# Optimization experiments

Measured on AMD Instinct MI355X. Metric: run time of the kernel, lower is better.

## Reference

```python
import jax, jax.numpy as jnp
import numpy as np

C, S, D, H, FF = 8, 512, 512, 8, 2048
DH = D // H
N = C * S
NUM_SAMPLES = 4
SEG_LEN = N // NUM_SAMPLES  # 2 channels * 512 tokens per sample


def _ln(x, w, b):
    m = x.mean(-1, keepdims=True)
    v = ((x - m) ** 2).mean(-1, keepdims=True)
    return (x - m) / jnp.sqrt(v + 1e-5) * w + b


def _rope_1d(t, p, inv_freq):
    # t: (H, N, hd), p: (N,), inv_freq: (hd//2,)
    f = p[:, None] * inv_freq[None, :]          # (N, hd//2)
    emb = jnp.concatenate([f, f], -1)           # (N, hd)
    cos, sin = jnp.cos(emb), jnp.sin(emb)
    half = t.shape[-1] // 2
    rot = jnp.concatenate([-t[..., half:], t[..., :half]], -1)
    return t * cos + rot * sin


def setup_inputs() -> dict:
    key = jax.random.key(0)
    ks = jax.random.split(key, 8)
    s = 0.02
    return {
        "x": jax.random.normal(ks[0], (C, S, D), jnp.float32),
        "pos": jax.random.uniform(ks[1], (C, S, 2), jnp.float32) * 100.0,
        "mask": jnp.zeros((C, S), jnp.bool_),
        "seg_ids": jnp.arange(N, dtype=jnp.int32),
        "Wqkv": jax.random.normal(ks[2], (D, 3 * D), jnp.float32) * s,
        "bqkv": jnp.zeros((3 * D,), jnp.float32),
        "Wo": jax.random.normal(ks[3], (D, D), jnp.float32) * s,
        "bo": jnp.zeros((D,), jnp.float32),
        "ln1_w": jnp.ones((D,), jnp.float32),
        "ln1_b": jnp.zeros((D,), jnp.float32),
        "ln2_w": jnp.ones((D,), jnp.float32),
        "ln2_b": jnp.zeros((D,), jnp.float32),
        "W1": jax.random.normal(ks[4], (D, FF), jnp.float32) * s,
        "b1": jnp.zeros((FF,), jnp.float32),
        "W2": jax.random.normal(ks[5], (FF, D), jnp.float32) * s,
        "b2": jnp.zeros((D,), jnp.float32),
    }


def reference(x, pos, mask, seg_ids, Wqkv, bqkv, Wo, bo,
              ln1_w, ln1_b, ln2_w, ln2_b, W1, b1, W2, b2):
    # Zero-mask forward_cc path: all C*S tokens are packed into one varlen batch.
    xf = x.reshape(N, D)
    pf = pos.reshape(N, 2)
    seg = seg_ids // SEG_LEN  # segment id per token (cu_seq_len semantics)

    # --- pre-LN MHA with 2D axial RoPE ---
    hn = _ln(xf, ln1_w, ln1_b)
    qkv = hn @ Wqkv + bqkv
    q, k, v = jnp.split(qkv, 3, axis=-1)
    to_heads = lambda t: t.reshape(N, H, DH).transpose(1, 0, 2)  # (H, N, DH)
    q, k, v = to_heads(q), to_heads(k), to_heads(v)

    hd2 = DH // 2
    inv_freq = 1.0 / (10000.0 ** (jnp.arange(0, hd2, 2, dtype=jnp.float32) / hd2))

    def rope2d(t):
        a = _rope_1d(t[..., :hd2], pf[:, 0], inv_freq)
        b = _rope_1d(t[..., hd2:], pf[:, 1], inv_freq)
        return jnp.concatenate([a, b], -1)

    q, k = rope2d(q), rope2d(k)

    scores = jnp.einsum('hnd,hmd->hnm', q, k) / np.float32(np.sqrt(DH))
    allowed = seg[:, None] == seg[None, :]  # block-diagonal varlen mask
    scores = jnp.where(allowed[None], scores, jnp.float32(-1e30))
    attn = jax.nn.softmax(scores, axis=-1)
    o = jnp.einsum('hnm,hmd->hnd', attn, v).transpose(1, 0, 2).reshape(N, D)
    h = xf + (o @ Wo + bo)

    # --- pre-LN FFN ---
    hn2 = _ln(h, ln2_w, ln2_b)
    h = h + (jax.nn.gelu(hn2 @ W1 + b1) @ W2 + b2)
    return h.reshape(C, S, D)
```

## Files before the change

kernel.cpp:

```cpp
#include <hip/hip_runtime.h>
#include <hip/hip_bf16.h>


typedef __hip_bfloat16 bf16;
typedef float f4 __attribute__((ext_vector_type(4)));
typedef short short8 __attribute__((ext_vector_type(8)));

#define C_ 8
#define S_ 512
#define D_ 512
#define H_ 8
#define DH_ 64
#define FF_ 2048
#define N_ 4096
#define SEGLEN 1024

__device__ __forceinline__ float bfbits2f(unsigned short u) {
    return __uint_as_float(((unsigned)u) << 16);
}
__device__ __forceinline__ unsigned short f2bfbits(float f) {
    __hip_bfloat16 h = __float2bfloat16(f);
    return *reinterpret_cast<unsigned short*>(&h);
}
__device__ __forceinline__ float in_get(const void* p, int i, int isbf) {
    return isbf ? bfbits2f(((const unsigned short*)p)[i]) : ((const float*)p)[i];
}
__device__ __forceinline__ int probe_bf(const void* ln1w) {
    return ((const unsigned*)ln1w)[0] != 0x3F800000u;
}
__device__ __forceinline__ float gelu_f(float x) {
    float u = 0.7978845608028654f * fmaf(0.044715f * x, x * x, x);
    return x * __builtin_amdgcn_rcpf(1.0f + __expf(-2.0f * u));
}
__device__ __forceinline__ void gl2lds16(const void* g, void* l) {
    __builtin_amdgcn_global_load_lds(
        (const __attribute__((address_space(1))) void*)g,
        (__attribute__((address_space(3))) void*)l, 16, 0, 0);
}

__device__ __forceinline__ void ln_row(
    const void* in, const void* w, const void* b, unsigned short* out,
    int isbf, int row, int lane, int in_fp32)
{
    int base = row * D_ + lane * 8;
    float v[8];
    if (in_fp32 || !isbf) {
        const f4* p = (const f4*)((const float*)in + base);
        f4 x0 = p[0], x1 = p[1];
        v[0] = x0[0]; v[1] = x0[1]; v[2] = x0[2]; v[3] = x0[3];
        v[4] = x1[0]; v[5] = x1[1]; v[6] = x1[2]; v[7] = x1[3];
    } else {
        uint4 u = *(const uint4*)((const unsigned short*)in + base);
        unsigned uu[4] = {u.x, u.y, u.z, u.w};
        #pragma unroll
        for (int j = 0; j < 4; j++) {
            v[2 * j]     = __uint_as_float(uu[j] << 16);
            v[2 * j + 1] = __uint_as_float(uu[j] & 0xFFFF0000u);
        }
    }
    float s = 0.f, q = 0.f;
    #pragma unroll
    for (int j = 0; j < 8; j++) { s += v[j]; q = fmaf(v[j], v[j], q); }
    #pragma unroll
    for (int m = 32; m; m >>= 1) { s += __shfl_xor(s, m); q += __shfl_xor(q, m); }
    float mean = s * (1.f / D_);
    float var  = q * (1.f / D_) - mean * mean;
    float rstd = rsqrtf(var + 1e-5f);
    unsigned short o[8];
    #pragma unroll
    for (int j = 0; j < 8; j++) {
        float wj = in_get(w, lane * 8 + j, isbf);
        float bj = in_get(b, lane * 8 + j, isbf);
        o[j] = f2bfbits((v[j] - mean) * rstd * wj + bj);
    }
    uint4 uo;
    uo.x = o[0] | ((unsigned)o[1] << 16);
    uo.y = o[2] | ((unsigned)o[3] << 16);
    uo.z = o[4] | ((unsigned)o[5] << 16);
    uo.w = o[6] | ((unsigned)o[7] << 16);
    *(uint4*)(out + base) = uo;
}

__device__ __forceinline__ void wtile_transpose(
    const void* __restrict__ src, bf16* __restrict__ dst, int K, int N,
    int nt, int kt, int isbf, unsigned short* t2)
{
    int nb = nt * 64, kb = kt * 32;
    #pragma unroll
    for (int pass = 0; pass < 2; pass++) {
        int k = pass * 16 + (threadIdx.x >> 4);
        int n = (threadIdx.x & 15) * 4;
        size_t gidx = (size_t)(kb + k) * N + nb + n;
        unsigned short v[4];
        if (!isbf) {
            f4 xv = *(const f4*)((const float*)src + gidx);
            v[0] = f2bfbits(xv[0]); v[1] = f2bfbits(xv[1]);
            v[2] = f2bfbits(xv[2]); v[3] = f2bfbits(xv[3]);
        } else {
            ushort4 u = *(const ushort4*)((const unsigned short*)src + gidx);
            v[0] = u.x; v[1] = u.y; v[2] = u.z; v[3] = u.w;
        }
        #pragma unroll
        for (int e = 0; e < 4; e++) t2[(n + e) * 40 + k] = v[e];
    }
    __syncthreads();
    int n = threadIdx.x >> 2, kc = (threadIdx.x & 3) * 8;
    uint4 w = *(const uint4*)&t2[n * 40 + kc];
    *(uint4*)&((unsigned short*)dst)[(size_t)(nb + n) * K + kb + kc] = w;
}

__global__ __launch_bounds__(256) void prep_kernel(
    const void* __restrict__ Wqkv, bf16* __restrict__ WqkvT,
    const void* __restrict__ x, const void* __restrict__ ln1w,
    const void* __restrict__ ln1b, unsigned short* __restrict__ hn)
{
    const int isbf = probe_bf(ln1w);
    __shared__ unsigned short t2[64 * 40];
    int b = blockIdx.x;
    if (b < 384) {
        wtile_transpose(Wqkv, WqkvT, 512, 1536, b % 24, b / 24, isbf, t2);
    } else {
        int row = (b - 384) * 4 + (threadIdx.x >> 6);
        ln_row(x, ln1w, ln1b, hn, isbf, row, threadIdx.x & 63, 0);
    }
}

__global__ __launch_bounds__(256) void ln_kernel(
    const void* __restrict__ in, const void* __restrict__ w, const void* __restrict__ b,
    unsigned short* __restrict__ out, const void* __restrict__ dtp, int in_fp32)
{
    const int isbf = probe_bf(dtp);
    int row = blockIdx.x * 4 + (threadIdx.x >> 6);
    ln_row(in, w, b, out, isbf, row, threadIdx.x & 63, in_fp32);
}

template<int MODE, int TM, int TN>
__global__ __launch_bounds__(256) void gemm_kernel(
    const bf16* __restrict__ A, const bf16* __restrict__ Bt,
    const void* __restrict__ bias, const void* __restrict__ res,
    const void* __restrict__ pos,
    void* __restrict__ out0, void* __restrict__ out1,
    int K, int NN, const void* __restrict__ dtp)
{
    const int isbf = probe_bf(dtp);
    constexpr int MI = TM / 32;
    constexpr int NT = TN / 32;
    constexpr int NB = TN / 32;
    constexpr int AS = TM * 64;
    constexpr int BS = TN * 64;
    constexpr int BUF = AS + BS;
    constexpr int VTSZ = 128 * 72;
    constexpr int SMSZ = (2 * BUF > VTSZ) ? 2 * BUF : VTSZ;
    __shared__ __align__(16) unsigned short smem[SMSZ];

    const int X = blockIdx.x & 7, jj = blockIdx.x >> 3;
    const int m0 = ((jj / NN) * 8 + X) * TM;
    const int n0 = (jj % NN) * TN;
    const int tid = threadIdx.x;
    const int wave = tid >> 6, lane = tid & 63;
    const int quad = lane >> 4, l16 = lane & 15;
    const int wr = wave >> 1, wc = wave & 1;

    const bf16* gA[MI]; int dA[MI];
    const bf16* gB[NB]; int dB[NB];
    #pragma unroll
    for (int j = 0; j < MI; j++) {
        int s = j * 256 + tid;
        int r = s >> 3, cc = ((s & 7) - r) & 7;
        gA[j] = A + (size_t)(m0 + r) * K + cc * 8;
        dA[j] = (j * 256 + wave * 64) * 8;
    }
    #pragma unroll
    for (int j = 0; j < NB; j++) {
        int s = j * 256 + tid;
        int r = s >> 3, cc = ((s & 7) - r) & 7;
        gB[j] = Bt + (size_t)(n0 + r) * K + cc * 8;
        dB[j] = (j * 256 + wave * 64) * 8;
    }
    auto stage = [&](int b, int kt) {
        unsigned short* Ab = smem + b * BUF;
        unsigned short* Bb = Ab + AS;
        #pragma unroll
        for (int j = 0; j < MI; j++) gl2lds16(gA[j] + kt * 64, Ab + dA[j]);
        #pragma unroll
        for (int j = 0; j < NB; j++) gl2lds16(gB[j] + kt * 64, Bb + dB[j]);
    };

    f4 acc[MI][NT] = {};
    const int nk = K >> 6;
    stage(0, 0);
    #pragma unroll 1
    for (int kt = 0; kt < nk; kt++) {
        const int cur = kt & 1;
        __syncthreads();
        if (kt + 1 < nk) stage(cur ^ 1, kt + 1);
        const unsigned short* Ab = smem + cur * BUF;
        const unsigned short* Bb = Ab + AS;
        short8 af[MI][2], bfr[NT][2];
        #pragma unroll
        for (int mi = 0; mi < MI; mi++) {
            int r = wr * (TM / 2) + mi * 16 + l16;
            #pragma unroll
            for (int h = 0; h < 2; h++)
                af[mi][h] = *(const short8*)&Ab[(r * 8 + ((h * 4 + quad + r) & 7)) * 8];
        }
        #pragma unroll
        for (int ni = 0; ni < NT; ni++) {
            int r = wc * (TN / 2) + ni * 16 + l16;
            #pragma unroll
            for (int h = 0; h < 2; h++)
                bfr[ni][h] = *(const short8*)&Bb[(r * 8 + ((h * 4 + quad + r) & 7)) * 8];
        }
        #pragma unroll
        for (int mi = 0; mi < MI; mi++)
            #pragma unroll
            for (int ni = 0; ni < NT; ni++) {
                acc[mi][ni] = __builtin_amdgcn_mfma_f32_16x16x32_bf16(af[mi][0], bfr[ni][0], acc[mi][ni], 0, 0, 0);
                acc[mi][ni] = __builtin_amdgcn_mfma_f32_16x16x32_bf16(af[mi][1], bfr[ni][1], acc[mi][ni], 0, 0, 0);
            }
    }

    const int colbase = n0 + wc * (TN / 2);
    float bb[NT];
    #pragma unroll
    for (int ni = 0; ni < NT; ni++) bb[ni] = in_get(bias, colbase + ni * 16 + l16, isbf);

    if (MODE == 1) {
        const int tsel = colbase >> 9;
        const int hd = (colbase & 511) >> 6;
        if (tsel < 2) {
            unsigned short* out = (unsigned short*)out0 + ((size_t)(tsel * H_ + hd) * N_) * 64;
            const float invf = __expf(-(float)l16 * 0.5756462732485114f);
            const float qscale = (tsel == 0) ? 0.125f : 1.0f;
            #pragma unroll
            for (int half = 0; half < 2; half++) {
                #pragma unroll
                for (int mi = 0; mi < MI; mi++) {
                    #pragma unroll
                    for (int r = 0; r < 4; r++) {
                        int row = m0 + wr * (TM / 2) + mi * 16 + quad * 4 + r;
                        float p = in_get(pos, row * 2 + half, isbf);
                        float sn, cs;
                        __sincosf(p * invf, &sn, &cs);
                        float v0 = acc[mi][half * 2][r]     + bb[half * 2];
                        float v1 = acc[mi][half * 2 + 1][r] + bb[half * 2 + 1];
                        out[(size_t)row * 64 + half * 32 + l16]      = f2bfbits((v0 * cs - v1 * sn) * qscale);
                        out[(size_t)row * 64 + half * 32 + 16 + l16] = f2bfbits((v1 * cs + v0 * sn) * qscale);
                    }
                }
            }
        } else {
            __syncthreads();
            unsigned short* VT = smem;
            const int vd_blk = n0 - 1024;
            #pragma unroll
            for (int mi = 0; mi < MI; mi++)
                #pragma unroll
                for (int ni = 0; ni < NT; ni++) {
                    int vd = wc * 64 + ni * 16 + l16;
                    #pragma unroll
                    for (int r = 0; r < 4; r++) {
                        int tok = wr * (TM / 2) + mi * 16 + quad * 4 + r;
                        VT[vd * 72 + tok] = f2bfbits(acc[mi][ni][r] + bb[ni]);
                    }
                }
            __syncthreads();
            unsigned short* vt = (unsigned short*)out1;
            #pragma unroll
            for (int j = 0; j < 4; j++) {
                int cch = j * 256 + tid;
                int dim = cch >> 3, tc = cch & 7;
                uint4 v = *(const uint4*)&VT[dim * 72 + tc * 8];
                *(uint4*)&vt[(size_t)(vd_blk + dim) * N_ + m0 + tc * 8] = v;
            }
        }
    } else {
        #pragma unroll
        for (int mi = 0; mi < MI; mi++)
            #pragma unroll
            for (int ni = 0; ni < NT; ni++) {
                int col = colbase + ni * 16 + l16;
                #pragma unroll
                for (int r = 0; r < 4; r++) {
                    int row = m0 + wr * (TM / 2) + mi * 16 + quad * 4 + r;
                    float val = acc[mi][ni][r] + bb[ni];
                    if (MODE == 2) {
                        size_t idx = (size_t)row * D_ + col;
                        ((float*)out0)[idx] = val + in_get(res, idx, isbf);
                    } else if (MODE == 3) {
                        ((unsigned short*)out0)[(size_t)row * FF_ + col] = f2bfbits(gelu_f(val));
                    } else {
                        size_t idx = (size_t)row * D_ + col;
                        float o = val + ((const float*)res)[idx];
                        if (isbf) ((unsigned short*)out0)[idx] = f2bfbits(o);
                        else      ((float*)out0)[idx] = o;
                    }
                }
            }
    }
}

#define PSTR 136
__global__ __launch_bounds__(256) void attn_kernel(
    const unsigned short* __restrict__ QKb, const unsigned short* __restrict__ Vt,
    unsigned short* __restrict__ ob,
    const void* __restrict__ tWo, const void* __restrict__ tW1,
    const void* __restrict__ tW2,
    bf16* __restrict__ dWo, bf16* __restrict__ dW1, bf16* __restrict__ dW2,
    const void* __restrict__ dtp)
{
    __shared__ __align__(16) unsigned short Ksm[2][128 * 64];
    __shared__ __align__(16) unsigned short Psm[4][16 * PSTR];

    if ((int)blockIdx.x >= 512) {
        const int isbf = probe_bf(dtp);
        int t = blockIdx.x - 512;
        if (t < 128)      wtile_transpose(tWo, dWo, 512, 512,  t % 8,  t / 8,  isbf, Ksm[0]);
        else if (t < 640) wtile_transpose(tW1, dW1, 512, 2048, (t - 128) % 32, (t - 128) / 32, isbf, Ksm[0]);
        else              wtile_transpose(tW2, dW2, 2048, 512, (t - 640) % 8,  (t - 640) / 8,  isbf, Ksm[0]);
        return;
    }

    const int h = blockIdx.x & 7, jb = blockIdx.x >> 3;
    const int sg = jb >> 4, qt = jb & 15;
    const int tid = threadIdx.x;
    const int wave = tid >> 6, lane = tid & 63;
    const int quad = lane >> 4, l16 = lane & 15;
    const unsigned short* Qg = QKb + ((size_t)h * N_ + sg * SEGLEN + qt * 64 + wave * 16) * 64;
    const unsigned short* Kg = QKb + ((size_t)(H_ + h) * N_ + sg * SEGLEN) * 64;
    unsigned short* Pw = Psm[wave];

    const unsigned short* gK[4];
    int lKoff[4];
    #pragma unroll
    for (int j = 0; j < 4; j++) {
        int s = j * 256 + tid;
        int rk = s >> 3, ck = ((s & 7) - rk) & 7;
        gK[j] = Kg + (size_t)rk * 64 + ck * 8;
        lKoff[j] = (j * 256 + wave * 64) * 8;
    }
    const int swzK0 = (quad + l16) & 7;
    const int swzK1 = (4 + quad + l16) & 7;

    const unsigned short* Vp[4];
    #pragma unroll
    for (int dt = 0; dt < 4; dt++)
        Vp[dt] = Vt + (size_t)h * 64 * N_ + (size_t)(dt * 16 + l16) * N_
                    + sg * SEGLEN + quad * 8;

    short8 qf0 = *(const short8*)(Qg + l16 * 64 + quad * 8);
    short8 qf1 = *(const short8*)(Qg + l16 * 64 + 32 + quad * 8);

    f4 o_acc[4] = {};
    float l_part[4] = {0.f, 0.f, 0.f, 0.f};

    #pragma unroll
    for (int j = 0; j < 4; j++) gl2lds16(gK[j], &Ksm[0][lKoff[j]]);

    #pragma unroll 1
    for (int kt = 0; kt < SEGLEN / 128; kt++) {
        const int cur = kt & 1;
        __syncthreads();
        if (kt + 1 < SEGLEN / 128) {
            #pragma unroll
            for (int j = 0; j < 4; j++)
                gl2lds16(gK[j] + (size_t)(kt + 1) * 128 * 64, &Ksm[cur ^ 1][lKoff[j]]);
        }
        const unsigned short* Kb = Ksm[cur];

        f4 Sc[8] = {};
        #pragma unroll
        for (int t = 0; t < 8; t++) {
            int r = t * 16 + l16;
            short8 kf0 = *(const short8*)&Kb[(r * 8 + swzK0) * 8];
            short8 kf1 = *(const short8*)&Kb[(r * 8 + swzK1) * 8];
            Sc[t] = __builtin_amdgcn_mfma_f32_16x16x32_bf16(qf0, kf0, Sc[t], 0, 0, 0);
            Sc[t] = __builtin_amdgcn_mfma_f32_16x16x32_bf16(qf1, kf1, Sc[t], 0, 0, 0);
        }
        #pragma unroll
        for (int t = 0; t < 8; t++)
            #pragma unroll
            for (int r = 0; r < 4; r++) {
                float pe = __expf(Sc[t][r]);
                Sc[t][r] = pe;
                l_part[r] += pe;
            }
        #pragma unroll
        for (int t = 0; t < 8; t++)
            #pragma unroll
            for (int r = 0; r < 4; r++)
                Pw[(quad * 4 + r) * PSTR + t * 16 + l16] = f2bfbits(Sc[t][r]);
        short8 pf[4];
        #pragma unroll
        for (int kc = 0; kc < 4; kc++)
            pf[kc] = *(const short8*)&Pw[l16 * PSTR + kc * 32 + quad * 8];
        #pragma unroll
        for (int dt = 0; dt < 4; dt++) {
            #pragma unroll
            for (int kc = 0; kc < 4; kc++) {
                short8 vf = *(const short8*)(Vp[dt] + kt * 128 + kc * 32);
                o_acc[dt] = __builtin_amdgcn_mfma_f32_16x16x32_bf16(pf[kc], vf, o_acc[dt], 0, 0, 0);
            }
        }
    }

    #pragma unroll
    for (int r = 0; r < 4; r++) {
        float l = l_part[r];
        l += __shfl_xor(l, 1);
        l += __shfl_xor(l, 2);
        l += __shfl_xor(l, 4);
        l += __shfl_xor(l, 8);
        float inv = __builtin_amdgcn_rcpf(l);
        int n = sg * SEGLEN + qt * 64 + wave * 16 + quad * 4 + r;
        #pragma unroll
        for (int dt = 0; dt < 4; dt++)
            ob[(size_t)n * D_ + h * DH_ + dt * 16 + l16] = f2bfbits(o_acc[dt][r] * inv);
    }
}

extern "C" void kernel_launch(void* const* d_in, const int* in_sizes, int n_in,
                              void* d_out, int out_size, void* d_ws, size_t ws_size,
                              hipStream_t stream)
{
    const void* x    = d_in[0];
    const void* pos  = d_in[1];
    const void* Wqkv = d_in[4];
    const void* bqkv = d_in[5];
    const void* Wo   = d_in[6];
    const void* bo   = d_in[7];
    const void* ln1w = d_in[8];
    const void* ln1b = d_in[9];
    const void* ln2w = d_in[10];
    const void* ln2b = d_in[11];
    const void* W1   = d_in[12];
    const void* b1   = d_in[13];
    const void* W2   = d_in[14];
    const void* b2   = d_in[15];

    char* ws = (char*)d_ws;
    size_t off = 0;
    auto take = [&](size_t bytes) -> void* {
        void* p = ws + off;
        off += (bytes + 255) & ~(size_t)255;
        return p;
    };
    bf16* WqkvT           = (bf16*)take((size_t)1536 * 512 * 2);
    bf16* WoT             = (bf16*)take((size_t)512 * 512 * 2);
    bf16* W1T             = (bf16*)take((size_t)2048 * 512 * 2);
    bf16* W2T             = (bf16*)take((size_t)512 * 2048 * 2);
    unsigned short* hn    = (unsigned short*)take((size_t)N_ * D_ * 2);
    unsigned short* QKb   = (unsigned short*)take((size_t)2 * H_ * N_ * DH_ * 2);
    unsigned short* Vtb   = (unsigned short*)take((size_t)H_ * DH_ * N_ * 2);
    unsigned short* obuf  = (unsigned short*)take((size_t)N_ * D_ * 2);
    float* hbuf           = (float*)take((size_t)N_ * D_ * 4);
    unsigned short* hn2   = (unsigned short*)take((size_t)N_ * D_ * 2);
    unsigned short* g     = (unsigned short*)take((size_t)N_ * FF_ * 2);

    prep_kernel<<<1408, 256, 0, stream>>>(Wqkv, WqkvT, x, ln1w, ln1b, hn);

    gemm_kernel<1, 64, 128><<<768, 256, 0, stream>>>(
        (const bf16*)hn, WqkvT, bqkv, nullptr, pos, QKb, Vtb, 512, 12, ln1w);

    attn_kernel<<<1664, 256, 0, stream>>>(
        QKb, Vtb, obuf, Wo, W1, W2, WoT, W1T, W2T, ln1w);

    gemm_kernel<2, 32, 64><<<1024, 256, 0, stream>>>(
        (const bf16*)obuf, WoT, bo, x, nullptr, hbuf, nullptr, 512, 8, ln1w);

    ln_kernel<<<N_ / 4, 256, 0, stream>>>(hbuf, ln2w, ln2b, hn2, ln1w, 1);

    gemm_kernel<3, 64, 64><<<2048, 256, 0, stream>>>(
        (const bf16*)hn2, W1T, b1, nullptr, nullptr, g, nullptr, 512, 32, ln1w);

    gemm_kernel<4, 32, 64><<<1024, 256, 0, stream>>>(
        (const bf16*)g, W2T, b2, hbuf, nullptr, d_out, nullptr, 2048, 8, ln1w);
}
```

Before: 205.9 us.

## Fuse second LayerNorm into FFN1 GEMM with a dedicated kernel

Removes the standalone ln_kernel and the hn2 buffer. A new ffn1_kernel recomputes LayerNorm for its 32-row A tile straight from the fp32 residual buffer into a swizzled LDS panel, then runs a 32x64 bf16 MFMA GEMM with double-buffered B tiles and a GELU epilogue. This saves one launch and the bf16 round trip for hn2. In exchange, every one of the 32 column blocks per row tile re-reads fp32 rows and recomputes the same LayerNorm, and the smaller tile gives each wave little MFMA work per k-step.

After: 424.6 us. +106.2%, slower.

```diff
diff --git a/kernel.cpp b/kernel.cpp
--- a/kernel.cpp
+++ b/kernel.cpp
@@ -123,15 +123,6 @@
         int row = (b - 384) * 4 + (threadIdx.x >> 6);
         ln_row(x, ln1w, ln1b, hn, isbf, row, threadIdx.x & 63, 0);
     }
-}
-
-__global__ __launch_bounds__(256) void ln_kernel(
-    const void* __restrict__ in, const void* __restrict__ w, const void* __restrict__ b,
-    unsigned short* __restrict__ out, const void* __restrict__ dtp, int in_fp32)
-{
-    const int isbf = probe_bf(dtp);
-    int row = blockIdx.x * 4 + (threadIdx.x >> 6);
-    ln_row(in, w, b, out, isbf, row, threadIdx.x & 63, in_fp32);
 }
 
 template<int MODE, int TM, int TN>
@@ -300,6 +291,108 @@
     }
 }
 
+__global__ __launch_bounds__(256) void ffn1_kernel(
+    const float* __restrict__ hb, const bf16* __restrict__ W1t,
+    const void* __restrict__ b1, const void* __restrict__ lnw,
+    const void* __restrict__ lnb, unsigned short* __restrict__ g,
+    const void* __restrict__ dtp)
+{
+    const int isbf = probe_bf(dtp);
+    __shared__ __align__(16) unsigned short Ap[32 * 512];
+    __shared__ __align__(16) unsigned short Bsm[2][64 * 64];
+
+    const int X = blockIdx.x & 7, jj = blockIdx.x >> 3;
+    const int m0 = ((jj >> 5) * 8 + X) * 32;
+    const int n0 = (jj & 31) * 64;
+    const int tid = threadIdx.x;
+    const int wave = tid >> 6, lane = tid & 63;
+    const int quad = lane >> 4, l16 = lane & 15;
+    const int wr = wave >> 1, wc = wave & 1;
+
+    const bf16* gB[2]; int dB[2];
+    #pragma unroll
+    for (int j = 0; j < 2; j++) {
+        int s = j * 256 + tid;
+        int rB = s >> 3, cB = ((s & 7) - rB) & 7;
+        gB[j] = W1t + (size_t)(n0 + rB) * 512 + cB * 8;
+        dB[j] = (j * 256 + wave * 64) * 8;
+    }
+    #pragma unroll
+    for (int j = 0; j < 2; j++) gl2lds16(gB[j], &Bsm[0][dB[j]]);
+
+    #pragma unroll 2
+    for (int i = 0; i < 8; i++) {
+        int r = wave * 8 + i;
+        const f4* p = (const f4*)(hb + (size_t)(m0 + r) * D_ + lane * 8);
+        f4 x0 = p[0], x1 = p[1];
+        float v[8] = {x0[0], x0[1], x0[2], x0[3], x1[0], x1[1], x1[2], x1[3]};
+        float s = 0.f, q = 0.f;
+        #pragma unroll
+        for (int j = 0; j < 8; j++) { s += v[j]; q = fmaf(v[j], v[j], q); }
+        #pragma unroll
+        for (int m = 32; m; m >>= 1) { s += __shfl_xor(s, m); q += __shfl_xor(q, m); }
+        float mean = s * (1.f / D_);
+        float rstd = rsqrtf(q * (1.f / D_) - mean * mean + 1e-5f);
+        unsigned short o[8];
+        #pragma unroll
+        for (int j = 0; j < 8; j++) {
+            float wj = in_get(lnw, lane * 8 + j, isbf);
+            float bj = in_get(lnb, lane * 8 + j, isbf);
+            o[j] = f2bfbits((v[j] - mean) * rstd * wj + bj);
+        }
+        uint4 uo;
+        uo.x = o[0] | ((unsigned)o[1] << 16);
+        uo.y = o[2] | ((unsigned)o[3] << 16);
+        uo.z = o[4] | ((unsigned)o[5] << 16);
+        uo.w = o[6] | ((unsigned)o[7] << 16);
+        *(uint4*)&Ap[r * 512 + ((lane + r) & 63) * 8] = uo;
+    }
+
+    f4 acc[2] = {};
+    #pragma unroll 1
+    for (int kt = 0; kt < 8; kt++) {
+        const int cur = kt & 1;
+        __syncthreads();
+        if (kt + 1 < 8) {
+            #pragma unroll
+            for (int j = 0; j < 2; j++)
+                gl2lds16(gB[j] + (kt + 1) * 64, &Bsm[cur ^ 1][dB[j]]);
+        }
+        const int rA = wr * 16 + l16;
+        short8 af[2];
+        #pragma unroll
+        for (int h = 0; h < 2; h++) {
+            int c = kt * 8 + h * 4 + quad;
+            af[h] = *(const short8*)&Ap[rA * 512 + ((c + rA) & 63) * 8];
+        }
+        short8 bfr[2][2];
+        #pragma unroll
+        for (int ni = 0; ni < 2; ni++) {
+            int rb = wc * 32 + ni * 16 + l16;
+            #pragma unroll
+            for (int h = 0; h < 2; h++)
+                bfr[ni][h] = *(const short8*)&Bsm[cur][(rb * 8 + ((h * 4 + quad + rb) & 7)) * 8];
+        }
+        #pragma unroll
+        for (int ni = 0; ni < 2; ni++) {
+            acc[ni] = __builtin_amdgcn_mfma_f32_16x16x32_bf16(af[0], bfr[ni][0], acc[ni], 0, 0, 0);
+            acc[ni] = __builtin_amdgcn_mfma_f32_16x16x32_bf16(af[1], bfr[ni][1], acc[ni], 0, 0, 0);
+        }
+    }
+
+    const int colbase = n0 + wc * 32;
+    #pragma unroll
+    for (int ni = 0; ni < 2; ni++) {
+        int col = colbase + ni * 16 + l16;
+        float bbv = in_get(b1, col, isbf);
+        #pragma unroll
+        for (int r = 0; r < 4; r++) {
+            int row = m0 + wr * 16 + quad * 4 + r;
+            g[(size_t)row * FF_ + col] = f2bfbits(gelu_f(acc[ni][r] + bbv));
+        }
+    }
+}
+
 #define PSTR 136
 __global__ __launch_bounds__(256) void attn_kernel(
     const unsigned short* __restrict__ QKb, const unsigned short* __restrict__ Vt,
@@ -454,7 +547,6 @@
     unsigned short* Vtb   = (unsigned short*)take((size_t)H_ * DH_ * N_ * 2);
     unsigned short* obuf  = (unsigned short*)take((size_t)N_ * D_ * 2);
     float* hbuf           = (float*)take((size_t)N_ * D_ * 4);
-    unsigned short* hn2   = (unsigned short*)take((size_t)N_ * D_ * 2);
     unsigned short* g     = (unsigned short*)take((size_t)N_ * FF_ * 2);
 
     prep_kernel<<<1408, 256, 0, stream>>>(Wqkv, WqkvT, x, ln1w, ln1b, hn);
@@ -468,10 +560,8 @@
     gemm_kernel<2, 32, 64><<<1024, 256, 0, stream>>>(
         (const bf16*)obuf, WoT, bo, x, nullptr, hbuf, nullptr, 512, 8, ln1w);
 
-    ln_kernel<<<N_ / 4, 256, 0, stream>>>(hbuf, ln2w, ln2b, hn2, ln1w, 1);
-
-    gemm_kernel<3, 64, 64><<<2048, 256, 0, stream>>>(
-        (const bf16*)hn2, W1T, b1, nullptr, nullptr, g, nullptr, 512, 32, ln1w);
+    ffn1_kernel<<<4096, 256, 0, stream>>>(
+        hbuf, W1T, b1, ln2w, ln2b, g, ln1w);
 
     gemm_kernel<4, 32, 64><<<1024, 256, 0, stream>>>(
         (const bf16*)g, W2T, b2, hbuf, nullptr, d_out, nullptr, 2048, 8, ln1w);
```
